# Kernel tuning notes

Measured on AMD Instinct MI355X. Metric: run time of the kernel, lower is better.

The kernel has to match this reference:

```python
import jax, jax.numpy as jnp
import numpy as np

B, S, H, F, E, TOP_K = 8, 1024, 1024, 3584, 8, 2


def setup_inputs() -> dict:
    key = jax.random.key(0)
    ks = jax.random.split(key, 10)
    hidden_states = jax.random.normal(ks[0], (B, S, H), jnp.float32)
    gate_w = jax.random.normal(ks[1], (E, H), jnp.float32) * 0.02
    # int8 weights stored as int-valued fp32 (symmetric quantized), per-output-channel scales
    w1_q = jnp.round(jnp.clip(jax.random.normal(ks[2], (E, F, H)) * 40.0, -127.0, 127.0))
    w1_s = jax.random.uniform(ks[3], (E, F), minval=1e-4, maxval=1e-3)
    w3_q = jnp.round(jnp.clip(jax.random.normal(ks[4], (E, F, H)) * 40.0, -127.0, 127.0))
    w3_s = jax.random.uniform(ks[5], (E, F), minval=1e-4, maxval=1e-3)
    w2_q = jnp.round(jnp.clip(jax.random.normal(ks[6], (E, H, F)) * 40.0, -127.0, 127.0))
    w2_s = jax.random.uniform(ks[7], (E, H), minval=1e-4, maxval=1e-3)
    # static per-expert input scale for the down projection (W8A8...WithQuantScale)
    down_scale = jax.random.uniform(ks[8], (E,), minval=0.01, maxval=0.05)
    return {"hidden_states": hidden_states, "gate_w": gate_w,
            "w1_q": w1_q, "w1_s": w1_s, "w3_q": w3_q, "w3_s": w3_s,
            "w2_q": w2_q, "w2_s": w2_s, "down_scale": down_scale}


def _quant_per_token(x):
    # symmetric per-token dynamic int8 quantization (act_quant='per-token')
    s = jnp.maximum(jnp.max(jnp.abs(x), axis=-1, keepdims=True), 1e-8) / 127.0
    q = jnp.clip(jnp.round(x / s), -127.0, 127.0)
    return q, s


def reference(hidden_states, gate_w, w1_q, w1_s, w3_q, w3_s, w2_q, w2_s, down_scale):
    b, s, h = hidden_states.shape
    x = hidden_states.reshape(b * s, h)              # [T, H]
    # --- router: softmax over experts, top-2, renormalize ---
    router_logits = x @ gate_w.T                     # [T, E]
    probs = jax.nn.softmax(router_logits.astype(jnp.float32), axis=-1)
    top_w, top_idx = jax.lax.top_k(probs, TOP_K)     # [T, 2]
    top_w = top_w / jnp.sum(top_w, axis=-1, keepdims=True)
    T = x.shape[0]
    # dense [T, E] routing weights (zero for unselected experts)
    w_dense = jnp.zeros((T, E), probs.dtype).at[jnp.arange(T)[:, None], top_idx].add(top_w)
    # --- quantize activations once (expert-independent per-token quant) ---
    x_q, x_s = _quant_per_token(x)
    out = jnp.zeros((T, h), jnp.float32)
    for e in range(E):  # fixed small expert count
        h1 = (x_q @ w1_q[e].T) * x_s * w1_s[e]       # [T, F] dequantized gate proj
        h3 = (x_q @ w3_q[e].T) * x_s * w3_s[e]       # [T, F] dequantized up proj
        g = jax.nn.silu(h1) * h3                     # SwiGLU
        g_q = jnp.clip(jnp.round(g / down_scale[e]), -127.0, 127.0)  # static-scale quant
        y = (g_q @ w2_q[e].T) * (down_scale[e] * w2_s[e])            # [T, H]
        out = out + w_dense[:, e:e + 1] * y
    return out.reshape(b, s, h), router_logits
```

## Files before the change

kernel.cpp:

```cpp
#include <hip/hip_runtime.h>
#include <stdint.h>

typedef int v4i  __attribute__((ext_vector_type(4)));
typedef int v16i __attribute__((ext_vector_type(16)));

#define T_TOK 8192
#define H_DIM 1024
#define F_DIM 3584
#define N_EXP 8

#define W13T_OFF  0u
#define XQ_OFF    58720256u
#define W2T_OFF   67108864u
#define GBT_OFF   96501760u
#define XS_OFF    158892032u
#define LIST_OFF  158924800u
#define TW_OFF    159186944u
#define TSLOT_OFF 159449088u
#define CNT_OFF   159514624u
#define OFFS_OFF  159514656u
#define NT_OFF    159514688u
#define WLIST_OFF 159514752u
#define RINFO_OFF 96501760u
#define WP_OFF    96534528u
#define BHIST_OFF 96600064u
#define XG_OFF    67108864u
#define XSG_OFF   84934656u
#define YBUF_OFF  0u

__device__ __forceinline__ void async16(const void* g, void* l) {
    __builtin_amdgcn_global_load_lds(
        (const __attribute__((address_space(1))) unsigned int*)g,
        (__attribute__((address_space(3))) unsigned int*)l, 16, 0, 0);
}

__device__ __forceinline__ int pack4(float a, float b, float c, float d) {
    int ia = (int)(signed char)(int)a, ib = (int)(signed char)(int)b;
    int ic = (int)(signed char)(int)c, id = (int)(signed char)(int)d;
    return (ia & 0xff) | ((ib & 0xff) << 8) | ((ic & 0xff) << 16) | (id << 24);
}

__global__ __launch_bounds__(256) void convert13_kernel(
    const float* __restrict__ w1, const float* __restrict__ w3,
    v4i* __restrict__ w13t)
{
    int d = blockIdx.x * 256 + threadIdx.x;
    int wi = d & 511;
    int rg = wi >> 7, c16 = (wi >> 5) & 3, r = wi & 31;
    int si = d >> 9;
    int mat = si & 1, kt = (si >> 1) & 15, rest = si >> 5;
    int e = rest / 28, ft = rest - e * 28;
    const float* s = (mat ? w3 : w1)
      + ((size_t)(e * F_DIM + ft * 128 + rg * 32 + r)) * H_DIM
      + kt * 64 + c16 * 16;
    const float4* sv = (const float4*)s;
    float4 f0 = sv[0], f1 = sv[1], f2 = sv[2], f3 = sv[3];
    v4i o;
    o.x = pack4(f0.x, f0.y, f0.z, f0.w);
    o.y = pack4(f1.x, f1.y, f1.z, f1.w);
    o.z = pack4(f2.x, f2.y, f2.z, f2.w);
    o.w = pack4(f3.x, f3.y, f3.z, f3.w);
    w13t[d] = o;
}

__global__ __launch_bounds__(256) void convert2_kernel(
    const float* __restrict__ w2, v4i* __restrict__ w2t)
{
    int d = blockIdx.x * 256 + threadIdx.x;
    int wi = d & 511;
    int rg = wi >> 7, c16 = (wi >> 5) & 3, r = wi & 31;
    int si = d >> 9;
    int kt = si % 56, q = si / 56;
    int ht = q & 7, e = q >> 3;
    const float* s = w2 + ((size_t)(e * H_DIM + ht * 128 + rg * 32 + r)) * F_DIM
          + kt * 64 + c16 * 16;
    const float4* sv = (const float4*)s;
    float4 f0 = sv[0], f1 = sv[1], f2 = sv[2], f3 = sv[3];
    v4i o;
    o.x = pack4(f0.x, f0.y, f0.z, f0.w);
    o.y = pack4(f1.x, f1.y, f1.z, f1.w);
    o.z = pack4(f2.x, f2.y, f2.z, f2.w);
    o.w = pack4(f3.x, f3.y, f3.z, f3.w);
    w2t[d] = o;
}

__global__ __launch_bounds__(256, 4) void router_kernel(
    const float* __restrict__ x, const float* __restrict__ gw,
    int8_t* __restrict__ xq, float* __restrict__ xs,
    int* __restrict__ bhist, int* __restrict__ rinfo, float2* __restrict__ wp,
    float* __restrict__ logits_out)
{
    const int t = threadIdx.x, lane = t & 63, wv = t >> 6;
    __shared__ int lhist[8];
    if (t < 8) lhist[t] = 0;
    __syncthreads();
    const float4* gw4 = (const float4*)gw;
#pragma unroll 1
    for (int i = 0; i < 2; i++) {
        const int token = blockIdx.x * 8 + wv * 2 + i;
        const float4* xrow = (const float4*)(x + (size_t)token * H_DIM);
        float4 xv[4];
#pragma unroll
        for (int j = 0; j < 4; j++) xv[j] = xrow[j * 64 + lane];
        float am = 0.0f;
#pragma unroll
        for (int j = 0; j < 4; j++)
            am = fmaxf(am, fmaxf(fmaxf(fabsf(xv[j].x), fabsf(xv[j].y)),
                                 fmaxf(fabsf(xv[j].z), fabsf(xv[j].w))));
        float l[8];
#pragma unroll
        for (int e = 0; e < 8; e++) {
            float d = 0.0f;
#pragma unroll
            for (int j = 0; j < 4; j++) {
                float4 g = gw4[e * 256 + j * 64 + lane];
                d += xv[j].x * g.x + xv[j].y * g.y + xv[j].z * g.z + xv[j].w * g.w;
            }
            l[e] = d;
        }
#pragma unroll
        for (int m = 1; m < 64; m <<= 1) {
#pragma unroll
            for (int e = 0; e < 8; e++) l[e] += __shfl_xor(l[e], m, 64);
            am = fmaxf(am, __shfl_xor(am, m, 64));
        }
        float v0 = l[0]; int i0 = 0;
#pragma unroll
        for (int e = 1; e < 8; e++) if (l[e] > v0) { v0 = l[e]; i0 = e; }
        float v1 = -3.4e38f; int i1 = 0;
#pragma unroll
        for (int e = 0; e < 8; e++) if (e != i0 && l[e] > v1) { v1 = l[e]; i1 = e; }
        const float tt = __expf(v1 - v0);
        const float w0 = 1.0f / (1.0f + tt);
        const float w1 = tt * w0;
        const float s = fmaxf(am, 1e-8f) / 127.0f;
        const float rs = 1.0f / s;
        int8_t* xqr = xq + (size_t)token * H_DIM;
#pragma unroll
        for (int j = 0; j < 4; j++) {
            char4 c;
            c.x = (signed char)fminf(fmaxf(rintf(xv[j].x * rs), -127.0f), 127.0f);
            c.y = (signed char)fminf(fmaxf(rintf(xv[j].y * rs), -127.0f), 127.0f);
            c.z = (signed char)fminf(fmaxf(rintf(xv[j].z * rs), -127.0f), 127.0f);
            c.w = (signed char)fminf(fmaxf(rintf(xv[j].w * rs), -127.0f), 127.0f);
            ((char4*)xqr)[j * 64 + lane] = c;
        }
        if (lane == 0) {
            xs[token] = s;
#pragma unroll
            for (int e = 0; e < 8; e++) logits_out[(size_t)token * 8 + e] = l[e];
            int r0 = atomicAdd(&lhist[i0], 1);
            int r1 = atomicAdd(&lhist[i1], 1);
            rinfo[token] = i0 | (i1 << 3) | (r0 << 6) | (r1 << 10);
            wp[token] = make_float2(w0, w1);
        }
    }
    __syncthreads();
    if (t < 8) bhist[blockIdx.x * 8 + t] = lhist[t];
}

__global__ __launch_bounds__(256) void planner_kernel(
    int* __restrict__ bhist, int* __restrict__ cnt, int* __restrict__ offs,
    int* __restrict__ ntile, int* __restrict__ wlist)
{
    __shared__ int sm[8 * 1060];
    __shared__ int tot[8];
    const int t = threadIdx.x;
#pragma unroll
    for (int k = 0; k < 32; k++) {
        int idx = k * 256 + t;
        int v = bhist[idx];
        int e = idx & 7, b = idx >> 3;
        sm[e * 1060 + b + (b >> 5)] = v;
    }
    __syncthreads();
    const int e = t >> 5, sub = t & 31;
    int* seg = sm + e * 1060 + sub * 33;
    int run = 0;
#pragma unroll
    for (int i = 0; i < 32; i++) { int v = seg[i]; seg[i] = run; run += v; }
    int inc = run;
#pragma unroll
    for (int d = 1; d < 32; d <<= 1) {
        int u = __shfl_up(inc, d, 32);
        if (sub >= d) inc += u;
    }
    const int segbase = inc - run;
    if (sub == 31) tot[e] = inc;
#pragma unroll
    for (int i = 0; i < 32; i++) seg[i] += segbase;
    __syncthreads();
    if (t == 0) {
        int s = 0, nt = 0;
        for (int ee = 0; ee < 8; ee++) {
            offs[ee] = s;
            int c = tot[ee];
            cnt[ee] = c;
            s += c;
            int tc = (c + 127) >> 7;
            for (int m = 0; m < tc; m++) wlist[nt++] = (ee << 8) | m;
        }
        *ntile = nt;
    }
#pragma unroll
    for (int k = 0; k < 32; k++) {
        int idx = k * 256 + t;
        int ee = idx & 7, b = idx >> 3;
        bhist[idx] = sm[ee * 1060 + b + (b >> 5)];
    }
}

__global__ __launch_bounds__(256) void scatter_kernel(
    const int* __restrict__ bhist, const int* __restrict__ rinfo,
    const float2* __restrict__ wp, int* __restrict__ list,
    float* __restrict__ tw, int* __restrict__ tslot)
{
    const int token = blockIdx.x * 256 + threadIdx.x;
    const int ri = rinfo[token];
    const float2 wpr = wp[token];
    const int b = token >> 3;
    const int e0 = ri & 7, e1 = (ri >> 3) & 7;
    const int r0 = (ri >> 6) & 15, r1 = (ri >> 10) & 15;
    const int p0 = bhist[b * 8 + e0] + r0;
    const int p1 = bhist[b * 8 + e1] + r1;
    list[e0 * T_TOK + p0] = token;  tw[e0 * T_TOK + p0] = wpr.x;
    list[e1 * T_TOK + p1] = token;  tw[e1 * T_TOK + p1] = wpr.y;
    tslot[token * 2 + 0] = (e0 << 16) | p0;
    tslot[token * 2 + 1] = (e1 << 16) | p1;
}

__global__ __launch_bounds__(256) void gather_kernel(
    const int8_t* __restrict__ xq, const float* __restrict__ xs,
    const int* __restrict__ cnt, const int* __restrict__ ntile_p,
    const int* __restrict__ wlist, const int* __restrict__ list,
    v4i* __restrict__ xg, float* __restrict__ xsg)
{
    const int bx = blockIdx.x;
    if (bx >= *ntile_p) return;
    const int wl = wlist[bx];
    const int e = wl >> 8, mt = wl & 255;
    const int count = cnt[e];
    const int cm1 = count - 1;
    const int t = threadIdx.x;
    const int* liste = list + e * T_TOK;
    __shared__ int stok[128];
    if (t < 128) {
        int p = mt * 128 + t;
        int tok = liste[p < count ? p : cm1];
        stok[t] = tok;
        xsg[bx * 128 + t] = xs[tok];
    }
    __syncthreads();
    v4i* dslab = xg + (size_t)bx * 8192;
#pragma unroll
    for (int i = 0; i < 32; i++) {
        int flat = i * 256 + t;
        int row = flat >> 6, c = flat & 63;
        v4i v = ((const v4i*)(xq + (size_t)stok[row] * H_DIM))[c];
        int kt = c >> 2, c16 = c & 3, rg = row >> 5, r = row & 31;
        dslab[kt * 512 + rg * 128 + c16 * 32 + r] = v;
    }
}

__global__ __launch_bounds__(256, 2) void gemm1_kernel(
    const v4i* __restrict__ xg, const float* __restrict__ xsg,
    const v4i* __restrict__ w13t,
    const float* __restrict__ w1s, const float* __restrict__ w3s,
    const float* __restrict__ dscale,
    const int* __restrict__ cnt, const int* __restrict__ ntile_p,
    const int* __restrict__ wlist,
    int8_t* __restrict__ gbt)
{
    const int h = blockIdx.x + blockIdx.y * 136;
    const int w476 = h >> 3;
    const int ft  = w476 / 17;
    const int bxi = w476 - ft * 17;
    const int bx  = (h & 7) * 17 + bxi;
    if (bx >= *ntile_p) return;
    const int wl = wlist[bx];
    const int e = wl >> 8, mt = wl & 255;
    const int count = cnt[e];
    const int t = threadIdx.x, lane = t & 63, w = t >> 6;
    const int wm = w >> 1, wn = w & 1;

    __shared__ v4i sm[4608];
    char* smb = (char*)sm;

    const char* gA = (const char*)(xg + (size_t)bx * 8192) + w * 2048 + lane * 16;
    const char* gB = (const char*)(w13t + (size_t)(e * 28 + ft) * 16384) + lane * 16;
    const int wq = w * 2048;

    v16i acc1[2][2], acc3[2][2];
#pragma unroll
    for (int i = 0; i < 2; i++)
#pragma unroll
        for (int j = 0; j < 2; j++)
#pragma unroll
            for (int r = 0; r < 16; r++) { acc1[i][j][r] = 0; acc3[i][j][r] = 0; }

    auto stage = [&](int kt, int buf) {
        char* base = smb + buf * 24576;
        const char* sa = gA + kt * 8192;
        async16(sa,        base + wq);
        async16(sa + 1024, base + wq + 1024);
        const char* s1 = gB + (size_t)kt * 16384;
        async16(s1 + wq,               base + 8192 + wq);
        async16(s1 + wq + 1024,        base + 8192 + wq + 1024);
        async16(s1 + 8192 + wq,        base + 16384 + wq);
        async16(s1 + 8192 + wq + 1024, base + 16384 + wq + 1024);
    };
    auto compute = [&](int buf) {
        const v4i* S = sm + buf * 1536;
#pragma unroll
        for (int ks = 0; ks < 2; ks++) {
            const int base = (2 * ks + (lane >> 5)) * 32 + (lane & 31);
            v4i a0  = S[base + (wm * 2 + 0) * 128];
            v4i a1  = S[base + (wm * 2 + 1) * 128];
            v4i b1a = S[512 + base + (wn * 2 + 0) * 128];
            v4i b1b = S[512 + base + (wn * 2 + 1) * 128];
            v4i b3a = S[1024 + base + (wn * 2 + 0) * 128];
            v4i b3b = S[1024 + base + (wn * 2 + 1) * 128];
            acc1[0][0] = __builtin_amdgcn_mfma_i32_32x32x32_i8(a0, b1a, acc1[0][0], 0, 0, 0);
            acc1[0][1] = __builtin_amdgcn_mfma_i32_32x32x32_i8(a0, b1b, acc1[0][1], 0, 0, 0);
            acc1[1][0] = __builtin_amdgcn_mfma_i32_32x32x32_i8(a1, b1a, acc1[1][0], 0, 0, 0);
            acc1[1][1] = __builtin_amdgcn_mfma_i32_32x32x32_i8(a1, b1b, acc1[1][1], 0, 0, 0);
            acc3[0][0] = __builtin_amdgcn_mfma_i32_32x32x32_i8(a0, b3a, acc3[0][0], 0, 0, 0);
            acc3[0][1] = __builtin_amdgcn_mfma_i32_32x32x32_i8(a0, b3b, acc3[0][1], 0, 0, 0);
            acc3[1][0] = __builtin_amdgcn_mfma_i32_32x32x32_i8(a1, b3a, acc3[1][0], 0, 0, 0);
            acc3[1][1] = __builtin_amdgcn_mfma_i32_32x32x32_i8(a1, b3b, acc3[1][1], 0, 0, 0);
        }
    };

    stage(0, 0);
    stage(1, 1);
    int bufc = 0, bufs = 2;
    for (int kt = 0; kt < 15; kt++) {
        asm volatile("s_waitcnt vmcnt(6)" ::: "memory");
        __builtin_amdgcn_s_barrier();
        if (kt + 2 < 16) stage(kt + 2, bufs);
        compute(bufc);
        bufc = (bufc == 2) ? 0 : bufc + 1;
        bufs = (bufs == 2) ? 0 : bufs + 1;
    }
    asm volatile("s_waitcnt vmcnt(0)" ::: "memory");
    __builtin_amdgcn_s_barrier();
    compute(bufc);

    const float ds = dscale[e];
    const float rds = 1.0f / ds;
    int8_t* gout = gbt + (size_t)bx * 458752 + (size_t)(ft * 2 + wn) * 8192;
#pragma unroll
    for (int im = 0; im < 2; im++) {
#pragma unroll
        for (int in = 0; in < 2; in++) {
            const int fco = in * 32 + (lane & 31);
            const int fcol = ft * 128 + wn * 64 + fco;
            const float s1 = w1s[e * F_DIM + fcol];
            const float s3 = w3s[e * F_DIM + fcol];
            const int coff = ((in * 2 + ((lane & 31) >> 4)) * 32) * 16 + (lane & 15);
#pragma unroll
            for (int r = 0; r < 16; r++) {
                int row = wm * 64 + im * 32 + (r & 3) + 8 * (r >> 2) + 4 * (lane >> 5);
                int p = mt * 128 + row;
                if (p < count) {
                    float sx = xsg[bx * 128 + row];
                    float h1 = (float)acc1[im][in][r] * sx * s1;
                    float h3 = (float)acc3[im][in][r] * sx * s3;
                    float g = h1 * __builtin_amdgcn_rcpf(1.0f + __expf(-h1)) * h3;
                    float qv = fminf(fmaxf(rintf(g * rds), -127.0f), 127.0f);
                    gout[(size_t)((wm * 2 + im) * 128 + (row & 31)) * 16 + coff] = (int8_t)qv;
                }
            }
        }
    }
}

__global__ __launch_bounds__(256, 3) void gemm2_kernel(
    const int8_t* __restrict__ gbt, const v4i* __restrict__ w2t,
    const float* __restrict__ w2s, const float* __restrict__ dscale,
    const int* __restrict__ cnt, const int* __restrict__ offs,
    const int* __restrict__ ntile_p, const int* __restrict__ wlist,
    const float* __restrict__ tw, float* __restrict__ ybuf)
{
    const int h = blockIdx.x + blockIdx.y * 136;
    const int wk = (h & 7) * 136 + (h >> 3);
    const int bx = wk >> 3;
    const int ht = wk & 7;
    if (bx >= *ntile_p) return;
    const int wl = wlist[bx];
    const int e = wl >> 8, mt = wl & 255;
    const int count = cnt[e];
    const int t = threadIdx.x, lane = t & 63, w = t >> 6;
    const int wm = w >> 1, wn = w & 1;

    __shared__ v4i sm[3072];
    char* smb = (char*)sm;

    const char* gA = (const char*)gbt + (size_t)bx * 458752 + w * 2048 + lane * 16;
    const char* gB = (const char*)(w2t + (size_t)(e * 8 + ht) * 28672) + w * 2048 + lane * 16;

    v16i acc[2][2];
#pragma unroll
    for (int i = 0; i < 2; i++)
#pragma unroll
        for (int j = 0; j < 2; j++)
#pragma unroll
            for (int r = 0; r < 16; r++) acc[i][j][r] = 0;

    auto stage = [&](int kt, int buf) {
        char* base = smb + buf * 16384;
        const size_t ko = (size_t)kt * 8192;
        async16(gA + ko,        base + w * 2048);
        async16(gA + ko + 1024, base + w * 2048 + 1024);
        async16(gB + ko,        base + 8192 + w * 2048);
        async16(gB + ko + 1024, base + 8192 + w * 2048 + 1024);
    };
    auto compute = [&](int buf) {
        const v4i* S = sm + buf * 1024;
#pragma unroll
        for (int ks = 0; ks < 2; ks++) {
            const int base = (2 * ks + (lane >> 5)) * 32 + (lane & 31);
            v4i a0 = S[base + (wm * 2 + 0) * 128];
            v4i a1 = S[base + (wm * 2 + 1) * 128];
            v4i b0 = S[512 + base + (wn * 2 + 0) * 128];
            v4i b1 = S[512 + base + (wn * 2 + 1) * 128];
            acc[0][0] = __builtin_amdgcn_mfma_i32_32x32x32_i8(a0, b0, acc[0][0], 0, 0, 0);
            acc[0][1] = __builtin_amdgcn_mfma_i32_32x32x32_i8(a0, b1, acc[0][1], 0, 0, 0);
            acc[1][0] = __builtin_amdgcn_mfma_i32_32x32x32_i8(a1, b0, acc[1][0], 0, 0, 0);
            acc[1][1] = __builtin_amdgcn_mfma_i32_32x32x32_i8(a1, b1, acc[1][1], 0, 0, 0);
        }
    };

    stage(0, 0);
    stage(1, 1);
    int bufc = 0, bufs = 2;
    for (int kt = 0; kt < 55; kt++) {
        asm volatile("s_waitcnt vmcnt(4)" ::: "memory");
        __builtin_amdgcn_s_barrier();
        if (kt + 2 < 56) stage(kt + 2, bufs);
        compute(bufc);
        bufc = (bufc == 2) ? 0 : bufc + 1;
        bufs = (bufs == 2) ? 0 : bufs + 1;
    }
    asm volatile("s_waitcnt vmcnt(0)" ::: "memory");
    __builtin_amdgcn_s_barrier();
    compute(bufc);

    const float ds = dscale[e];
    const int rowbase = offs[e] + mt * 128;
#pragma unroll
    for (int im = 0; im < 2; im++) {
#pragma unroll
        for (int in = 0; in < 2; in++) {
            const int h2 = ht * 128 + wn * 64 + in * 32 + (lane & 31);
            const float sc = ds * w2s[e * H_DIM + h2];
#pragma unroll
            for (int r = 0; r < 16; r++) {
                int row = wm * 64 + im * 32 + (r & 3) + 8 * (r >> 2) + 4 * (lane >> 5);
                int p = mt * 128 + row;
                if (p < count) {
                    float rw = tw[e * T_TOK + p];
                    ybuf[(size_t)(rowbase + row) * H_DIM + h2] = (float)acc[im][in][r] * sc * rw;
                }
            }
        }
    }
}

__global__ __launch_bounds__(256) void combine_kernel(
    const float* __restrict__ ybuf, const int* __restrict__ offs,
    const int* __restrict__ tslot, float* __restrict__ out)
{
    const int token = blockIdx.x;
    const int i = threadIdx.x;
    const int s0 = tslot[token * 2 + 0];
    const int s1 = tslot[token * 2 + 1];
    const int slot0 = offs[s0 >> 16] + (s0 & 0xffff);
    const int slot1 = offs[s1 >> 16] + (s1 & 0xffff);
    float4 a = ((const float4*)(ybuf + (size_t)slot0 * H_DIM))[i];
    float4 b = ((const float4*)(ybuf + (size_t)slot1 * H_DIM))[i];
    float4 o;
    o.x = a.x + b.x; o.y = a.y + b.y; o.z = a.z + b.z; o.w = a.w + b.w;
    ((float4*)(out + (size_t)token * H_DIM))[i] = o;
}

extern "C" void kernel_launch(void* const* d_in, const int* in_sizes, int n_in,
                              void* d_out, int out_size, void* d_ws, size_t ws_size,
                              hipStream_t stream)
{
    const float* x    = (const float*)d_in[0];
    const float* gw   = (const float*)d_in[1];
    const float* w1   = (const float*)d_in[2];
    const float* w1s  = (const float*)d_in[3];
    const float* w3   = (const float*)d_in[4];
    const float* w3s  = (const float*)d_in[5];
    const float* w2   = (const float*)d_in[6];
    const float* w2s  = (const float*)d_in[7];
    const float* dsc  = (const float*)d_in[8];

    float* out = (float*)d_out;
    float* logits_out = out + (size_t)T_TOK * H_DIM;

    char* ws = (char*)d_ws;
    v4i*    w13t = (v4i*)   (ws + W13T_OFF);
    int8_t* xq   = (int8_t*)(ws + XQ_OFF);
    v4i*    w2t  = (v4i*)   (ws + W2T_OFF);
    int8_t* gbt  = (int8_t*)(ws + GBT_OFF);
    float*  xs   = (float*) (ws + XS_OFF);
    int*    list = (int*)   (ws + LIST_OFF);
    float*  tws  = (float*) (ws + TW_OFF);
    int*    tslot= (int*)   (ws + TSLOT_OFF);
    int*    cnt  = (int*)   (ws + CNT_OFF);
    int*    offs = (int*)   (ws + OFFS_OFF);
    int*    ntile= (int*)   (ws + NT_OFF);
    int*    wlist= (int*)   (ws + WLIST_OFF);
    int*    rinfo= (int*)   (ws + RINFO_OFF);
    float2* wp   = (float2*)(ws + WP_OFF);
    int*    bhist= (int*)   (ws + BHIST_OFF);
    v4i*    xg   = (v4i*)   (ws + XG_OFF);
    float*  xsg  = (float*) (ws + XSG_OFF);
    float*  ybuf = (float*) (ws + YBUF_OFF);

    convert13_kernel<<<14336, 256, 0, stream>>>(w1, w3, w13t);
    router_kernel<<<1024, 256, 0, stream>>>(x, gw, xq, xs, bhist, rinfo, wp, logits_out);
    planner_kernel<<<1, 256, 0, stream>>>(bhist, cnt, offs, ntile, wlist);
    scatter_kernel<<<32, 256, 0, stream>>>(bhist, rinfo, wp, list, tws, tslot);
    gather_kernel<<<136, 256, 0, stream>>>(xq, xs, cnt, ntile, wlist, list, xg, xsg);
    gemm1_kernel<<<dim3(136, 28), 256, 0, stream>>>(
        xg, xsg, w13t, w1s, w3s, dsc, cnt, ntile, wlist, gbt);
    convert2_kernel<<<7168, 256, 0, stream>>>(w2, w2t);
    gemm2_kernel<<<dim3(136, 8), 256, 0, stream>>>(
        gbt, w2t, w2s, dsc, cnt, offs, ntile, wlist, tws, ybuf);
    combine_kernel<<<T_TOK, 256, 0, stream>>>(ybuf, offs, tslot, out);
}
```

Measured before the change: 733.4 us.

## Load A operand directly into registers, staging only B tiles through LDS

In both grouped GEMM kernels the activation (A) tile is no longer staged through shared memory. Each wave loads its own A fragments straight from global memory into registers one k-step ahead, and only the weight (B) tiles keep going through the async LDS ring. This shrinks LDS per block, which may allow more resident blocks, and cuts LDS read traffic for A. The costs are more VGPR pressure and direct global loads whose latency relies on the vmcnt accounting, so the wait counts were adjusted. Each A fragment is also fetched redundantly by the two waves that share a row block.

Result: slower. 786.3 us (+7.2%).

```diff
diff --git a/kernel.cpp b/kernel.cpp
--- a/kernel.cpp
+++ b/kernel.cpp
@@ -283,10 +283,11 @@
     const int t = threadIdx.x, lane = t & 63, w = t >> 6;
     const int wm = w >> 1, wn = w & 1;
 
-    __shared__ v4i sm[4608];
+    __shared__ v4i sm[3072];
     char* smb = (char*)sm;
 
-    const char* gA = (const char*)(xg + (size_t)bx * 8192) + w * 2048 + lane * 16;
+    const int aoff = ((lane >> 5) * 32) + (lane & 31) + wm * 256;
+    const v4i* gAv = xg + (size_t)bx * 8192 + aoff;
     const char* gB = (const char*)(w13t + (size_t)(e * 28 + ft) * 16384) + lane * 16;
     const int wq = w * 2048;
 
@@ -298,28 +299,25 @@
 #pragma unroll
             for (int r = 0; r < 16; r++) { acc1[i][j][r] = 0; acc3[i][j][r] = 0; }
 
-    auto stage = [&](int kt, int buf) {
-        char* base = smb + buf * 24576;
-        const char* sa = gA + kt * 8192;
-        async16(sa,        base + wq);
-        async16(sa + 1024, base + wq + 1024);
+    auto stageB = [&](int kt, int buf) {
+        char* base = smb + buf * 16384;
         const char* s1 = gB + (size_t)kt * 16384;
-        async16(s1 + wq,               base + 8192 + wq);
-        async16(s1 + wq + 1024,        base + 8192 + wq + 1024);
-        async16(s1 + 8192 + wq,        base + 16384 + wq);
-        async16(s1 + 8192 + wq + 1024, base + 16384 + wq + 1024);
+        async16(s1 + wq,               base + wq);
+        async16(s1 + wq + 1024,        base + wq + 1024);
+        async16(s1 + 8192 + wq,        base + 8192 + wq);
+        async16(s1 + 8192 + wq + 1024, base + 8192 + wq + 1024);
     };
-    auto compute = [&](int buf) {
-        const v4i* S = sm + buf * 1536;
+    auto computeR = [&](int buf, v4i a00, v4i a10, v4i a01, v4i a11) {
+        const v4i* S = sm + buf * 1024;
 #pragma unroll
         for (int ks = 0; ks < 2; ks++) {
             const int base = (2 * ks + (lane >> 5)) * 32 + (lane & 31);
-            v4i a0  = S[base + (wm * 2 + 0) * 128];
-            v4i a1  = S[base + (wm * 2 + 1) * 128];
-            v4i b1a = S[512 + base + (wn * 2 + 0) * 128];
-            v4i b1b = S[512 + base + (wn * 2 + 1) * 128];
-            v4i b3a = S[1024 + base + (wn * 2 + 0) * 128];
-            v4i b3b = S[1024 + base + (wn * 2 + 1) * 128];
+            v4i a0 = ks ? a10 : a00;
+            v4i a1 = ks ? a11 : a01;
+            v4i b1a = S[base + (wn * 2 + 0) * 128];
+            v4i b1b = S[base + (wn * 2 + 1) * 128];
+            v4i b3a = S[512 + base + (wn * 2 + 0) * 128];
+            v4i b3b = S[512 + base + (wn * 2 + 1) * 128];
             acc1[0][0] = __builtin_amdgcn_mfma_i32_32x32x32_i8(a0, b1a, acc1[0][0], 0, 0, 0);
             acc1[0][1] = __builtin_amdgcn_mfma_i32_32x32x32_i8(a0, b1b, acc1[0][1], 0, 0, 0);
             acc1[1][0] = __builtin_amdgcn_mfma_i32_32x32x32_i8(a1, b1a, acc1[1][0], 0, 0, 0);
@@ -331,20 +329,24 @@
         }
     };
 
-    stage(0, 0);
-    stage(1, 1);
+    v4i c00 = gAv[0], c10 = gAv[64], c01 = gAv[128], c11 = gAv[192];
+    stageB(0, 0);
+    stageB(1, 1);
+    v4i n00, n10, n01, n11;
     int bufc = 0, bufs = 2;
     for (int kt = 0; kt < 15; kt++) {
-        asm volatile("s_waitcnt vmcnt(6)" ::: "memory");
+        const v4i* gAn = gAv + (size_t)(kt + 1) * 512;
+        n00 = gAn[0]; n10 = gAn[64]; n01 = gAn[128]; n11 = gAn[192];
+        asm volatile("s_waitcnt vmcnt(8)" ::: "memory");
         __builtin_amdgcn_s_barrier();
-        if (kt + 2 < 16) stage(kt + 2, bufs);
-        compute(bufc);
+        if (kt + 2 < 16) { stageB(kt + 2, bufs); bufs = (bufs == 2) ? 0 : bufs + 1; }
+        computeR(bufc, c00, c10, c01, c11);
         bufc = (bufc == 2) ? 0 : bufc + 1;
-        bufs = (bufs == 2) ? 0 : bufs + 1;
+        c00 = n00; c10 = n10; c01 = n01; c11 = n11;
     }
     asm volatile("s_waitcnt vmcnt(0)" ::: "memory");
     __builtin_amdgcn_s_barrier();
-    compute(bufc);
+    computeR(bufc, c00, c10, c01, c11);
 
     const float ds = dscale[e];
     const float rds = 1.0f / ds;
@@ -393,11 +395,13 @@
     const int t = threadIdx.x, lane = t & 63, w = t >> 6;
     const int wm = w >> 1, wn = w & 1;
 
-    __shared__ v4i sm[3072];
+    __shared__ v4i sm[1536];
     char* smb = (char*)sm;
 
-    const char* gA = (const char*)gbt + (size_t)bx * 458752 + w * 2048 + lane * 16;
-    const char* gB = (const char*)(w2t + (size_t)(e * 8 + ht) * 28672) + w * 2048 + lane * 16;
+    const int aoff = ((lane >> 5) * 32) + (lane & 31) + wm * 256;
+    const v4i* gAv = (const v4i*)(gbt + (size_t)bx * 458752) + aoff;
+    const char* gB = (const char*)(w2t + (size_t)(e * 8 + ht) * 28672) + lane * 16;
+    const int wq = w * 2048;
 
     v16i acc[2][2];
 #pragma unroll
@@ -407,23 +411,21 @@
 #pragma unroll
             for (int r = 0; r < 16; r++) acc[i][j][r] = 0;
 
-    auto stage = [&](int kt, int buf) {
-        char* base = smb + buf * 16384;
-        const size_t ko = (size_t)kt * 8192;
-        async16(gA + ko,        base + w * 2048);
-        async16(gA + ko + 1024, base + w * 2048 + 1024);
-        async16(gB + ko,        base + 8192 + w * 2048);
-        async16(gB + ko + 1024, base + 8192 + w * 2048 + 1024);
+    auto stageB = [&](int kt, int buf) {
+        char* base = smb + buf * 8192;
+        const char* s1 = gB + (size_t)kt * 8192;
+        async16(s1 + wq,        base + wq);
+        async16(s1 + wq + 1024, base + wq + 1024);
     };
-    auto compute = [&](int buf) {
-        const v4i* S = sm + buf * 1024;
+    auto computeR = [&](int buf, v4i a00, v4i a10, v4i a01, v4i a11) {
+        const v4i* S = sm + buf * 512;
 #pragma unroll
         for (int ks = 0; ks < 2; ks++) {
             const int base = (2 * ks + (lane >> 5)) * 32 + (lane & 31);
-            v4i a0 = S[base + (wm * 2 + 0) * 128];
-            v4i a1 = S[base + (wm * 2 + 1) * 128];
-            v4i b0 = S[512 + base + (wn * 2 + 0) * 128];
-            v4i b1 = S[512 + base + (wn * 2 + 1) * 128];
+            v4i a0 = ks ? a10 : a00;
+            v4i a1 = ks ? a11 : a01;
+            v4i b0 = S[base + (wn * 2 + 0) * 128];
+            v4i b1 = S[base + (wn * 2 + 1) * 128];
             acc[0][0] = __builtin_amdgcn_mfma_i32_32x32x32_i8(a0, b0, acc[0][0], 0, 0, 0);
             acc[0][1] = __builtin_amdgcn_mfma_i32_32x32x32_i8(a0, b1, acc[0][1], 0, 0, 0);
             acc[1][0] = __builtin_amdgcn_mfma_i32_32x32x32_i8(a1, b0, acc[1][0], 0, 0, 0);
@@ -431,20 +433,24 @@
         }
     };
 
-    stage(0, 0);
-    stage(1, 1);
+    v4i c00 = gAv[0], c10 = gAv[64], c01 = gAv[128], c11 = gAv[192];
+    stageB(0, 0);
+    stageB(1, 1);
+    v4i n00, n10, n01, n11;
     int bufc = 0, bufs = 2;
     for (int kt = 0; kt < 55; kt++) {
-        asm volatile("s_waitcnt vmcnt(4)" ::: "memory");
+        const v4i* gAn = gAv + (size_t)(kt + 1) * 512;
+        n00 = gAn[0]; n10 = gAn[64]; n01 = gAn[128]; n11 = gAn[192];
+        asm volatile("s_waitcnt vmcnt(6)" ::: "memory");
         __builtin_amdgcn_s_barrier();
-        if (kt + 2 < 56) stage(kt + 2, bufs);
-        compute(bufc);
+        if (kt + 2 < 56) { stageB(kt + 2, bufs); bufs = (bufs == 2) ? 0 : bufs + 1; }
+        computeR(bufc, c00, c10, c01, c11);
         bufc = (bufc == 2) ? 0 : bufc + 1;
-        bufs = (bufs == 2) ? 0 : bufs + 1;
+        c00 = n00; c10 = n10; c01 = n01; c11 = n11;
     }
     asm volatile("s_waitcnt vmcnt(0)" ::: "memory");
     __builtin_amdgcn_s_barrier();
-    compute(bufc);
+    computeR(bufc, c00, c10, c01, c11);
 
     const float ds = dscale[e];
     const int rowbase = offs[e] + mt * 128;
```
